# Optimization experiments

Measured on AMD Instinct MI355X. Metric: run time of the kernel, lower is better.

The kernel has to match this reference:

```python
import jax, jax.numpy as jnp
import numpy as np

HEADS = 16

def setup_inputs() -> dict:
    key = jax.random.key(0)
    ks = jax.random.split(key, 5)
    B, T, D = 2, 2048, 2048
    s = 0.02
    return {
        "x": jax.random.normal(ks[0], (B, T, D), dtype=jnp.float32),
        "Wq": jax.random.normal(ks[1], (D, D), dtype=jnp.float32) * s,
        "Wk": jax.random.normal(ks[2], (D, D), dtype=jnp.float32) * s,
        "Wv": jax.random.normal(ks[3], (D, D), dtype=jnp.float32) * s,
        "Wo": jax.random.normal(ks[4], (D, D), dtype=jnp.float32) * s,
    }

def reference(x, Wq, Wk, Wv, Wo):
    B, T, _ = x.shape
    H = HEADS
    Dh = Wq.shape[1] // H
    # projections: [B,T,H,Dh]
    q = (x @ Wq).reshape(B, T, H, Dh)
    k = (x @ Wk).reshape(B, T, H, Dh)
    v = (x @ Wv).reshape(B, T, H, Dh)
    # raw scores [B,H,T,T]
    scores = jnp.einsum("bthd,bshd->bhts", q, k)
    # NOTE (faithful to source): mask is multiplicative 0/1 tril (the
    # masked_fill(-inf) in the torch code is not in-place and has no effect),
    # and the scale is sqrt(token_len), not sqrt(head_dim).
    mask = jnp.tril(jnp.ones((T, T), dtype=scores.dtype))
    scores = scores * mask
    attn = jax.nn.softmax(scores / (T ** 0.5), axis=-1)
    out = jnp.einsum("bhts,bshd->bthd", attn, v).reshape(B, T, H * Dh)
    return out @ Wo
```

## Files before the change

### kernel.cpp

```cpp
#include <hip/hip_runtime.h>


typedef __attribute__((ext_vector_type(4))) float  f32x4;
typedef __attribute__((ext_vector_type(8))) short  bf16x8;
typedef __attribute__((ext_vector_type(4))) unsigned short u16x4;

#define AS1 __attribute__((address_space(1)))
#define AS3 __attribute__((address_space(3)))

__device__ __forceinline__ void llds16(const void* g, void* l) {
  __builtin_amdgcn_global_load_lds((const AS1 void*)g, (AS3 void*)l, 16, 0, 0);
}

__device__ __forceinline__ unsigned short f2bf(float f) {
  unsigned int u = __builtin_bit_cast(unsigned int, f);
  u += 0x7fffu + ((u >> 16) & 1u);
  return (unsigned short)(u >> 16);
}

__device__ __forceinline__ unsigned short f2bfru(float f) {
  return (unsigned short)((__builtin_bit_cast(unsigned int, f) + 0x8000u) >> 16);
}

__device__ __forceinline__ float bf2f(unsigned short u) {
  return __builtin_bit_cast(float, (unsigned int)u << 16);
}

__global__ __launch_bounds__(256) void prep_kernel(
    const float* __restrict__ x,
    const float* __restrict__ W0, const float* __restrict__ W1,
    const float* __restrict__ W2, const float* __restrict__ W3,
    unsigned short* __restrict__ Xb,
    unsigned short* __restrict__ T0, unsigned short* __restrict__ T1,
    unsigned short* __restrict__ T2, unsigned short* __restrict__ T3) {
  __shared__ float tile[32][33];
  const int z = blockIdx.z;
  const int tx = threadIdx.x;
  const int ty = threadIdx.y;
  if (z == 4) {
    int blk = blockIdx.y * 64 + blockIdx.x;
    int t = (ty << 5) + tx;
    int i = blk * 512 + t;
#pragma unroll
    for (int c = 0; c < 2; ++c) {
      f32x4 v = ((const f32x4*)x)[i + (c << 8)];
      u16x4 o;
      o[0] = f2bf(v[0]); o[1] = f2bf(v[1]); o[2] = f2bf(v[2]); o[3] = f2bf(v[3]);
      ((u16x4*)Xb)[i + (c << 8)] = o;
    }
    return;
  }
  const float* W = (z == 0) ? W0 : (z == 1) ? W1 : (z == 2) ? W2 : W3;
  unsigned short* Wt = (z == 0) ? T0 : (z == 1) ? T1 : (z == 2) ? T2 : T3;
  const int bx = blockIdx.x << 5;
  const int by = blockIdx.y << 5;
#pragma unroll
  for (int r = ty; r < 32; r += 8)
    tile[r][tx] = W[(size_t)(bx + r) * 2048 + by + tx];
  __syncthreads();
#pragma unroll
  for (int r = ty; r < 32; r += 8)
    Wt[(size_t)(by + r) * 2048 + bx + tx] = f2bf(tile[tx][r]);
}

__global__ __launch_bounds__(512, 2) void gemm_qkv(const unsigned short* __restrict__ A,
                                                   const unsigned short* __restrict__ Bt,
                                                   unsigned short* __restrict__ Qb,
                                                   unsigned short* __restrict__ Kb,
                                                   unsigned short* __restrict__ Vt) {
  constexpr int SLOT = 49152;
  __shared__ __align__(16) char smem[3 * SLOT];
  const int tid  = threadIdx.x;
  const int lane = tid & 63;
  const int w    = tid >> 6;
  const int wr   = w >> 2;
  const int wc   = w & 3;
  const int q16  = lane >> 4;
  const int l15  = lane & 15;
  const int f    = blockIdx.x;
  const int g    = f >> 3;
  const int bn   = (f & 7) * 3 + (g % 3);
  const int bm   = g / 3;

  const int srow = tid >> 3;
  const int scl  = (tid & 7) ^ (srow & 7);
  const unsigned short* aS = A  + (size_t)((bm << 7) + srow) * 2048 + (scl << 3);
  const unsigned short* bS = Bt + (size_t)(bn * 256 + srow) * 2048 + (scl << 3);
  const int sdst = tid << 4;

  const int swzb = (q16 ^ (l15 & 7)) << 4;
  const int aRd  = ((wr << 6) + l15) << 7;

  f32x4 acc[4][4];
#pragma unroll
  for (int i = 0; i < 4; ++i)
#pragma unroll
    for (int j = 0; j < 4; ++j) acc[i][j] = (f32x4){0.f, 0.f, 0.f, 0.f};

  auto stageT = [&](int kt, char* sb) {
    const size_t ko = (size_t)kt << 6;
    llds16(aS + ko,               sb + sdst);
    llds16(aS + (64 * 2048) + ko, sb + 8192 + sdst);
#pragma unroll
    for (int r = 0; r < 4; ++r)
      llds16(bS + (size_t)r * (64 * 2048) + ko, sb + 16384 + (r << 13) + sdst);
  };

  auto computeT = [&](const char* base) {
#pragma unroll
    for (int ks = 0; ks < 2; ++ks) {
      const int sw = swzb ^ (ks << 6);
      bf16x8 af[4], bf[4];
#pragma unroll
      for (int mi = 0; mi < 4; ++mi)
        af[mi] = *(const bf16x8*)(base + aRd + (mi << 11) + sw);
#pragma unroll
      for (int ni = 0; ni < 4; ++ni)
        bf[ni] = *(const bf16x8*)(base + 16384 + (((wc << 6) + l15) << 7) + (ni << 11) + sw);
      __builtin_amdgcn_s_setprio(1);
#pragma unroll
      for (int mi = 0; mi < 4; ++mi)
#pragma unroll
        for (int ni = 0; ni < 4; ++ni)
          acc[mi][ni] = __builtin_amdgcn_mfma_f32_16x16x32_bf16(af[mi], bf[ni], acc[mi][ni], 0, 0, 0);
      __builtin_amdgcn_s_setprio(0);
    }
  };

  char* s0 = smem;
  char* s1 = smem + SLOT;
  char* s2 = smem + 2 * SLOT;

#define W6()  asm volatile("s_waitcnt vmcnt(6)" ::: "memory")
#define W0()  asm volatile("s_waitcnt vmcnt(0)" ::: "memory")
#define BAR() __builtin_amdgcn_s_barrier()

  stageT(0, s0); stageT(1, s1);
  W6(); BAR();
  stageT(2, s2);
  computeT(s0);
#pragma unroll 1
  for (int b = 1; b <= 25; b += 3) {
    W6(); BAR(); stageT(b + 2, s0); computeT(s1);
    W6(); BAR(); stageT(b + 3, s1); computeT(s2);
    W6(); BAR(); stageT(b + 4, s2); computeT(s0);
  }
  W6(); BAR(); stageT(30, s0); computeT(s1);
  W6(); BAR(); stageT(31, s1); computeT(s2);
  W6(); BAR(); computeT(s0);
  W0(); BAR(); computeT(s1);

#undef W6
#undef W0
#undef BAR

  const float qscale = 0.02209708691207961f;
  const int rb = q16 << 2;
#pragma unroll
  for (int mi = 0; mi < 4; ++mi) {
    int m0 = (bm << 7) + (wr << 6) + (mi << 4) + rb;
#pragma unroll
    for (int ni = 0; ni < 4; ++ni) {
      int gn = (bn << 8) + (wc << 6) + (ni << 4) + l15;
      int region = gn >> 11;
      int nloc = gn & 2047;
      if (region == 0) {
#pragma unroll
        for (int j = 0; j < 4; ++j)
          Qb[(size_t)(m0 + j) * 2048 + nloc] = f2bf(acc[mi][ni][j] * qscale);
      } else if (region == 1) {
#pragma unroll
        for (int j = 0; j < 4; ++j)
          Kb[(size_t)(m0 + j) * 2048 + nloc] = f2bf(acc[mi][ni][j]);
      } else {
        u16x4 pk;
#pragma unroll
        for (int j = 0; j < 4; ++j) pk[j] = f2bf(acc[mi][ni][j]);
        int b = m0 >> 11, t = m0 & 2047;
        *(u16x4*)(Vt + ((size_t)((b << 4) + (nloc >> 7)) * 128 + (nloc & 127)) * 2048 + t) = pk;
      }
    }
  }
}

__global__ __launch_bounds__(256, 2) void gemm_wo(const unsigned short* __restrict__ A,
                                                  const unsigned short* __restrict__ Bt,
                                                  float* __restrict__ Co) {
  constexpr int SLOT = 8192 + 8192;
  __shared__ __align__(16) char smem[3 * SLOT];

  const int tid  = threadIdx.x;
  const int lane = tid & 63;
  const int w    = tid >> 6;
  const int q16  = lane >> 4;
  const int l15  = lane & 15;
  const int f    = blockIdx.x;
  const int g    = f >> 3;
  const int bn   = ((f & 7) << 1) + (g & 1);
  const int bm   = g >> 1;
  const int wmb  = (w >> 1) << 6;
  const int wnb  = (w & 1) << 6;

  f32x4 acc[4][4];
#pragma unroll
  for (int i = 0; i < 4; ++i)
#pragma unroll
    for (int j = 0; j < 4; ++j) acc[i][j] = (f32x4){0.f, 0.f, 0.f, 0.f};

  const int rowA = tid >> 2;
  const int chA  = tid & 3;
  auto stageT = [&](int t, char* sb) {
    const int k0 = t << 5;
#pragma unroll
    for (int r = 0; r < 2; ++r) {
      int row = (r << 6) + rowA;
      const unsigned short* src = A + (size_t)((bm << 7) + row) * 2048 + k0
                                    + ((chA ^ ((row >> 1) & 3)) << 3);
      llds16(src, sb + (r << 12) + (w << 10));
    }
#pragma unroll
    for (int r = 0; r < 2; ++r) {
      int row = (r << 6) + rowA;
      const unsigned short* src = Bt + (size_t)((bn << 7) + row) * 2048 + k0
                                     + ((chA ^ ((row >> 1) & 3)) << 3);
      llds16(src, sb + 8192 + (r << 12) + (w << 10));
    }
  };

  auto computeT = [&](const char* base) {
    bf16x8 af[4], bf[4];
#pragma unroll
    for (int mi = 0; mi < 4; ++mi) {
      int row = wmb + (mi << 4) + l15;
      af[mi] = *(const bf16x8*)(base + (row << 6) + ((q16 ^ ((row >> 1) & 3)) << 4));
    }
#pragma unroll
    for (int ni = 0; ni < 4; ++ni) {
      int row = wnb + (ni << 4) + l15;
      bf[ni] = *(const bf16x8*)(base + 8192 + (row << 6) + ((q16 ^ ((row >> 1) & 3)) << 4));
    }
    __builtin_amdgcn_s_setprio(1);
#pragma unroll
    for (int mi = 0; mi < 4; ++mi)
#pragma unroll
      for (int ni = 0; ni < 4; ++ni)
        acc[mi][ni] = __builtin_amdgcn_mfma_f32_16x16x32_bf16(af[mi], bf[ni], acc[mi][ni], 0, 0, 0);
    __builtin_amdgcn_s_setprio(0);
  };

  auto STEP = [&](int t, char* cbase, char* sbase) {
    asm volatile("s_waitcnt vmcnt(4)" ::: "memory");
    __builtin_amdgcn_s_barrier();
    stageT(t + 2, sbase);
    computeT(cbase);
  };

  char* s0 = smem;
  char* s1 = smem + SLOT;
  char* s2 = smem + 2 * SLOT;

  stageT(0, s0); stageT(1, s1);
#pragma unroll 1
  for (int t = 0; t < 60; t += 3) {
    STEP(t,     s0, s2);
    STEP(t + 1, s1, s0);
    STEP(t + 2, s2, s1);
  }
  STEP(60, s0, s2);
  STEP(61, s1, s0);
  asm volatile("s_waitcnt vmcnt(4)" ::: "memory");
  __builtin_amdgcn_s_barrier();
  computeT(s2);
  asm volatile("s_waitcnt vmcnt(0)" ::: "memory");
  __builtin_amdgcn_s_barrier();
  computeT(s0);

  const int rb = q16 << 2;
#pragma unroll
  for (int mi = 0; mi < 4; ++mi) {
    int m0 = (bm << 7) + wmb + (mi << 4) + rb;
#pragma unroll
    for (int ni = 0; ni < 4; ++ni) {
      int n = (bn << 7) + wnb + (ni << 4) + l15;
#pragma unroll
      for (int j = 0; j < 4; ++j)
        Co[(size_t)(m0 + j) * 2048 + n] = acc[mi][ni][j];
    }
  }
}

__global__ __launch_bounds__(256) void vsuf_kernel(const unsigned short* __restrict__ Vt,
                                                   float* __restrict__ Suf) {
  const int row  = blockIdx.x * 4 + (threadIdx.x >> 6);
  const int lane = threadIdx.x & 63;
  const unsigned short* vp = Vt + (size_t)row * 2048 + (lane << 5);
  float a = 0.f;
#pragma unroll
  for (int c = 0; c < 4; ++c) {
    bf16x8 v = *(const bf16x8*)(vp + (c << 3));
#pragma unroll
    for (int j = 0; j < 8; ++j) a += bf2f((unsigned short)v[j]);
  }
  float I = a;
#pragma unroll
  for (int off = 1; off < 64; off <<= 1) {
    float t = __shfl_down(I, off, 64);
    I += (lane + off < 64) ? t : 0.f;
  }
  Suf[(size_t)lane * 4096 + row] = I;
  if (lane == 0) Suf[(size_t)64 * 4096 + row] = 0.f;
}

__global__ __launch_bounds__(256, 2) void attn_kernel(const unsigned short* __restrict__ Q,
                                                      const unsigned short* __restrict__ K,
                                                      const unsigned short* __restrict__ V,
                                                      const float* __restrict__ Suf,
                                                      unsigned short* __restrict__ O) {
  __shared__ __align__(16) char smem[57344];
  const int tid  = threadIdx.x;
  const int lane = tid & 63;
  const int w    = tid >> 6;
  const int q16  = lane >> 4;
  const int l15  = lane & 15;
  const int f    = blockIdx.x;
  const int bh   = ((f & 7) << 2) + ((f >> 3) & 3);
  const int fs   = f >> 5;
  const int strip = (fs < 8) ? (15 - fs) : (fs - 8);
  const int b  = bh >> 4;
  const size_t qkbase = ((size_t)(b << 11)) * 2048 + ((size_t)(bh & 15) << 7);
  const size_t vbase  = (size_t)bh << 18;
  const int rb = q16 << 2;
  char* Psm = smem + 49152 + (w << 11);

  const int numIter = 4 * strip + 4;
  const int t0 = (strip << 7) + (w << 5);

  auto stage = [&](int s0, int sb) {
#pragma unroll
    for (int c = 0; c < 2; ++c) {
      int ch = (w << 1) + c;
      int rowK = (ch << 2) + q16;
      int colbK = (l15 << 4) ^ ((rowK & 7) << 4);
      llds16(K + qkbase + (size_t)(s0 + rowK) * 2048 + (colbK >> 1), smem + sb + (ch << 10));
      int rowV = (ch << 4) + (lane >> 2);
      int colbV = ((lane & 3) << 4) ^ (((rowV >> 2) & 3) << 4);
      llds16(V + vbase + (size_t)rowV * 2048 + s0 + (colbV >> 1), smem + sb + 8192 + (ch << 10));
    }
  };

  bf16x8 qf[4], qg[4];
  {
    const unsigned short* qp = Q + qkbase + (size_t)(t0 + l15) * 2048 + (q16 << 3);
#pragma unroll
    for (int kk = 0; kk < 4; ++kk) qf[kk] = *(const bf16x8*)(qp + (kk << 5));
    const unsigned short* qp2 = qp + (size_t)16 * 2048;
#pragma unroll
    for (int kk = 0; kk < 4; ++kk) qg[kk] = *(const bf16x8*)(qp2 + (kk << 5));
  }

  f32x4 oA[8], oB[8];
#pragma unroll
  for (int i = 0; i < 8; ++i) { oA[i] = (f32x4){0.f,0.f,0.f,0.f}; oB[i] = (f32x4){0.f,0.f,0.f,0.f}; }
  float ellA[4] = {0.f,0.f,0.f,0.f}, ellB[4] = {0.f,0.f,0.f,0.f};

  stage(0, 0);
  stage(32, 16384);
  asm volatile("s_waitcnt vmcnt(4)" ::: "memory");
  __syncthreads();

  int cs = 0;
  for (int it = 0; it < numIter; ++it) {
    const int s0 = it << 5;
    const bool st = (it + 2 < numIter);
    if (st) {
      int ss = cs + 2; if (ss >= 3) ss -= 3;
      stage(s0 + 64, ss << 14);
    }

    if (s0 <= t0) {
      const int kb = cs << 14;
      const int vb = kb + 8192;

      f32x4 sA = (f32x4){0.f,0.f,0.f,0.f}, sB = sA, sC = sA, sD = sA;
#pragma unroll
      for (int kk = 0; kk < 4; ++kk) {
        int r0 = l15, r1 = 16 + l15;
        bf16x8 k0f = *(const bf16x8*)(smem + kb + (r0 << 8) + (((kk << 6) + (q16 << 4)) ^ ((r0 & 7) << 4)));
        bf16x8 k1f = *(const bf16x8*)(smem + kb + (r1 << 8) + (((kk << 6) + (q16 << 4)) ^ ((r1 & 7) << 4)));
        sA = __builtin_amdgcn_mfma_f32_16x16x32_bf16(qf[kk], k0f, sA, 0, 0, 0);
        sC = __builtin_amdgcn_mfma_f32_16x16x32_bf16(qg[kk], k0f, sC, 0, 0, 0);
        sB = __builtin_amdgcn_mfma_f32_16x16x32_bf16(qf[kk], k1f, sB, 0, 0, 0);
        sD = __builtin_amdgcn_mfma_f32_16x16x32_bf16(qg[kk], k1f, sD, 0, 0, 0);
      }

      float pA[4], pB[4], pC[4], pD[4];
      if (s0 + 32 <= t0) {
#pragma unroll
        for (int j = 0; j < 4; ++j) {
          pA[j] = __expf(sA[j]); pB[j] = __expf(sB[j]);
          pC[j] = __expf(sC[j]); pD[j] = __expf(sD[j]);
          ellA[j] += pA[j] + pB[j];
          ellB[j] += pC[j] + pD[j];
        }
      } else {
#pragma unroll
        for (int j = 0; j < 4; ++j) {
          int tA = t0 + rb + j, tB = tA + 16;
          int sa = s0 + l15;
          float vA = (sa <= tA)      ? sA[j] : 0.f;
          float vB = (sa + 16 <= tA) ? sB[j] : 0.f;
          float vC = (sa <= tB)      ? sC[j] : 0.f;
          float vD = (sa + 16 <= tB) ? sD[j] : 0.f;
          pA[j] = __expf(vA); pB[j] = __expf(vB);
          pC[j] = __expf(vC); pD[j] = __expf(vD);
          ellA[j] += pA[j] + pB[j];
          ellB[j] += pC[j] + pD[j];
        }
      }

#pragma unroll
      for (int j = 0; j < 4; ++j) {
        int rA = rb + j;
        int swzA = ((rA >> 1) & 3) << 4;
        *(unsigned short*)(Psm + (rA << 6) + ((l15 << 1) ^ swzA))        = f2bfru(pA[j]);
        *(unsigned short*)(Psm + (rA << 6) + ((32 + (l15 << 1)) ^ swzA)) = f2bfru(pB[j]);
        int rB = rA + 16;
        int swzB = ((rB >> 1) & 3) << 4;
        *(unsigned short*)(Psm + (rB << 6) + ((l15 << 1) ^ swzB))        = f2bfru(pC[j]);
        *(unsigned short*)(Psm + (rB << 6) + ((32 + (l15 << 1)) ^ swzB)) = f2bfru(pD[j]);
      }
      asm volatile("s_waitcnt lgkmcnt(0)" ::: "memory");

      bf16x8 paA, paB;
      {
        int r = l15;
        paA = *(const bf16x8*)(Psm + (r << 6) + ((q16 << 4) ^ (((r >> 1) & 3) << 4)));
        int r2 = 16 + l15;
        paB = *(const bf16x8*)(Psm + (r2 << 6) + ((q16 << 4) ^ (((r2 >> 1) & 3) << 4)));
      }
#pragma unroll
      for (int ni = 0; ni < 8; ++ni) {
        int dr = (ni << 4) + l15;
        bf16x8 vbf = *(const bf16x8*)(smem + vb + (dr << 6) + ((q16 << 4) ^ (((dr >> 2) & 3) << 4)));
        oA[ni] = __builtin_amdgcn_mfma_f32_16x16x32_bf16(paA, vbf, oA[ni], 0, 0, 0);
        oB[ni] = __builtin_amdgcn_mfma_f32_16x16x32_bf16(paB, vbf, oB[ni], 0, 0, 0);
      }
    }

    if (it + 1 < numIter) {
      if (st) asm volatile("s_waitcnt vmcnt(4)" ::: "memory");
      else    asm volatile("s_waitcnt vmcnt(0)" ::: "memory");
      __builtin_amdgcn_s_barrier();
    }
    cs = (cs + 1 == 3) ? 0 : cs + 1;
  }

  const int send = t0 + 32;
  const float* sp = Suf + (size_t)(send >> 5) * 4096 + ((size_t)bh << 7);
  const float extra = (float)(2048 - send);
#pragma unroll
  for (int ni = 0; ni < 8; ++ni) {
    float sv = sp[(ni << 4) + l15];
#pragma unroll
    for (int j = 0; j < 4; ++j) { oA[ni][j] += sv; oB[ni][j] += sv; }
  }

#pragma unroll
  for (int j = 0; j < 4; ++j) {
    float r = ellA[j];
    r += __shfl_xor(r, 1, 64);
    r += __shfl_xor(r, 2, 64);
    r += __shfl_xor(r, 4, 64);
    r += __shfl_xor(r, 8, 64);
    float inv = 1.0f / (r + extra);
    int t = t0 + rb + j;
    unsigned short* op = O + qkbase + (size_t)t * 2048;
#pragma unroll
    for (int ni = 0; ni < 8; ++ni)
      op[(ni << 4) + l15] = f2bf(oA[ni][j] * inv);

    float r2 = ellB[j];
    r2 += __shfl_xor(r2, 1, 64);
    r2 += __shfl_xor(r2, 2, 64);
    r2 += __shfl_xor(r2, 4, 64);
    r2 += __shfl_xor(r2, 8, 64);
    float inv2 = 1.0f / (r2 + extra);
    unsigned short* op2 = op + (size_t)16 * 2048;
#pragma unroll
    for (int ni = 0; ni < 8; ++ni)
      op2[(ni << 4) + l15] = f2bf(oB[ni][j] * inv2);
  }
}

extern "C" void kernel_launch(void* const* d_in, const int* in_sizes, int n_in,
                              void* d_out, int out_size, void* d_ws, size_t ws_size,
                              hipStream_t stream) {
  (void)in_sizes; (void)n_in; (void)out_size; (void)ws_size;
  const float* x  = (const float*)d_in[0];
  const float* Wq = (const float*)d_in[1];
  const float* Wk = (const float*)d_in[2];
  const float* Wv = (const float*)d_in[3];
  const float* Wo = (const float*)d_in[4];
  float* out = (float*)d_out;

  char* ws = (char*)d_ws;
  unsigned short* Xb  = (unsigned short*)(ws);
  unsigned short* Wqt = (unsigned short*)(ws + 16777216);
  unsigned short* Wkt = (unsigned short*)(ws + 16777216 + 8388608);
  unsigned short* Wvt = (unsigned short*)(ws + 16777216 + 2 * 8388608);
  unsigned short* Wot = (unsigned short*)(ws + 16777216 + 3 * 8388608);
  unsigned short* Qb  = (unsigned short*)(ws + 50331648);
  unsigned short* Kb  = (unsigned short*)(ws + 67108864);
  unsigned short* Vt  = (unsigned short*)(ws + 83886080);
  unsigned short* Ob  = Xb;
  float*          Suf = (float*)Wqt;

  {
    dim3 tb(32, 8), tg(64, 64, 5);
    prep_kernel<<<tg, tb, 0, stream>>>(x, Wq, Wk, Wv, Wo, Xb, Wqt, Wkt, Wvt, Wot);
  }
  gemm_qkv<<<768, 512, 0, stream>>>(Xb, Wqt, Qb, Kb, Vt);

  vsuf_kernel<<<1024, 256, 0, stream>>>(Vt, Suf);

  attn_kernel<<<512, 256, 0, stream>>>(Qb, Kb, Vt, Suf, Ob);

  gemm_wo<<<512, 256, 0, stream>>>(Ob, Wot, out);
}
```

Measured before the change: 260.6 us.

## Load V tiles directly into registers with double-buffered prefetch, shrink LDS

V tiles now go straight from global memory into registers through a two-slot register double buffer, instead of being staged into LDS and read back. Only K is still staged in LDS, which cuts shared memory from 56KB to 32KB. The main loop is manually unrolled by two so the two V register buffers can alternate. The aim is to remove LDS traffic and the V-tile LDS reads, and possibly to raise occupancy. In exchange, register pressure grows (16 extra bf16x8 vectors) and V global loads are per-lane strided rather than LDS-coalesced. The odd-count tail is handled implicitly, because numIter is always a multiple of 4.

```diff
diff --git a/kernel.cpp b/kernel.cpp
--- a/kernel.cpp
+++ b/kernel.cpp
@@ -316,7 +316,7 @@
                                                       const unsigned short* __restrict__ V,
                                                       const float* __restrict__ Suf,
                                                       unsigned short* __restrict__ O) {
-  __shared__ __align__(16) char smem[57344];
+  __shared__ __align__(16) char smem[32768];
   const int tid  = threadIdx.x;
   const int lane = tid & 63;
   const int w    = tid >> 6;
@@ -328,25 +328,30 @@
   const int strip = (fs < 8) ? (15 - fs) : (fs - 8);
   const int b  = bh >> 4;
   const size_t qkbase = ((size_t)(b << 11)) * 2048 + ((size_t)(bh & 15) << 7);
-  const size_t vbase  = (size_t)bh << 18;
   const int rb = q16 << 2;
-  char* Psm = smem + 49152 + (w << 11);
+  char* Psm = smem + 24576 + (w << 11);
 
   const int numIter = 4 * strip + 4;
   const int t0 = (strip << 7) + (w << 5);
 
-  auto stage = [&](int s0, int sb) {
-#pragma unroll
-    for (int c = 0; c < 2; ++c) {
-      int ch = (w << 1) + c;
-      int rowK = (ch << 2) + q16;
-      int colbK = (l15 << 4) ^ ((rowK & 7) << 4);
-      llds16(K + qkbase + (size_t)(s0 + rowK) * 2048 + (colbK >> 1), smem + sb + (ch << 10));
-      int rowV = (ch << 4) + (lane >> 2);
-      int colbV = ((lane & 3) << 4) ^ (((rowV >> 2) & 3) << 4);
-      llds16(V + vbase + (size_t)rowV * 2048 + s0 + (colbV >> 1), smem + sb + 8192 + (ch << 10));
-    }
-  };
+  const unsigned short* vSrc = V + ((size_t)bh << 18) + (size_t)l15 * 2048 + (q16 << 3);
+
+#define LOADV(S0_, D)  do {                                                  \
+    _Pragma("unroll")                                                        \
+    for (int ni = 0; ni < 8; ++ni)                                           \
+      D[ni] = *(const bf16x8*)(vSrc + (size_t)ni * 32768 + (S0_));           \
+  } while (0)
+
+#define STAGEK(S0_, SB) do {                                                 \
+    _Pragma("unroll")                                                        \
+    for (int c = 0; c < 2; ++c) {                                            \
+      int ch = (w << 1) + c;                                                 \
+      int rowK = (ch << 2) + q16;                                            \
+      int colbK = (l15 << 4) ^ ((rowK & 7) << 4);                            \
+      llds16(K + qkbase + (size_t)((S0_) + rowK) * 2048 + (colbK >> 1),      \
+             (SB) + (ch << 10));                                             \
+    }                                                                        \
+  } while (0)
 
   bf16x8 qf[4], qg[4];
   {
@@ -362,98 +367,107 @@
 #pragma unroll
   for (int i = 0; i < 8; ++i) { oA[i] = (f32x4){0.f,0.f,0.f,0.f}; oB[i] = (f32x4){0.f,0.f,0.f,0.f}; }
   float ellA[4] = {0.f,0.f,0.f,0.f}, ellB[4] = {0.f,0.f,0.f,0.f};
-
-  stage(0, 0);
-  stage(32, 16384);
-  asm volatile("s_waitcnt vmcnt(4)" ::: "memory");
+  bf16x8 vA[8], vB[8];
+
+#define TILE(T, KSLOT, KSTG, VUSE, VLD) do {                                 \
+    const int s0_ = (T) << 5;                                                \
+    const bool hasNext_  = ((T) + 1 < numIter);                              \
+    const bool hasStage_ = ((T) + 2 < numIter);                              \
+    if (hasNext_)  LOADV(s0_ + 32, VLD);                                     \
+    if (hasStage_) STAGEK(s0_ + 64, KSTG);                                   \
+    if (s0_ <= t0) {                                                         \
+      const char* kb_ = (KSLOT);                                             \
+      f32x4 sA = (f32x4){0.f,0.f,0.f,0.f}, sB = sA, sC = sA, sD = sA;        \
+      _Pragma("unroll")                                                      \
+      for (int kk = 0; kk < 4; ++kk) {                                       \
+        int r0 = l15, r1 = 16 + l15;                                         \
+        bf16x8 k0f = *(const bf16x8*)(kb_ + (r0 << 8) +                      \
+                     (((kk << 6) + (q16 << 4)) ^ ((r0 & 7) << 4)));          \
+        bf16x8 k1f = *(const bf16x8*)(kb_ + (r1 << 8) +                      \
+                     (((kk << 6) + (q16 << 4)) ^ ((r1 & 7) << 4)));          \
+        sA = __builtin_amdgcn_mfma_f32_16x16x32_bf16(qf[kk], k0f, sA, 0, 0, 0); \
+        sC = __builtin_amdgcn_mfma_f32_16x16x32_bf16(qg[kk], k0f, sC, 0, 0, 0); \
+        sB = __builtin_amdgcn_mfma_f32_16x16x32_bf16(qf[kk], k1f, sB, 0, 0, 0); \
+        sD = __builtin_amdgcn_mfma_f32_16x16x32_bf16(qg[kk], k1f, sD, 0, 0, 0); \
+      }                                                                      \
+      float pA[4], pB[4], pC[4], pD[4];                                      \
+      if (s0_ + 32 <= t0) {                                                  \
+        _Pragma("unroll")                                                    \
+        for (int j = 0; j < 4; ++j) {                                        \
+          pA[j] = __expf(sA[j]); pB[j] = __expf(sB[j]);                      \
+          pC[j] = __expf(sC[j]); pD[j] = __expf(sD[j]);                      \
+          ellA[j] += pA[j] + pB[j];                                          \
+          ellB[j] += pC[j] + pD[j];                                          \
+        }                                                                    \
+      } else {                                                               \
+        _Pragma("unroll")                                                    \
+        for (int j = 0; j < 4; ++j) {                                        \
+          int tA = t0 + rb + j, tB = tA + 16;                                \
+          int sa = s0_ + l15;                                                \
+          float vA_ = (sa <= tA)      ? sA[j] : 0.f;                         \
+          float vB_ = (sa + 16 <= tA) ? sB[j] : 0.f;                         \
+          float vC_ = (sa <= tB)      ? sC[j] : 0.f;                         \
+          float vD_ = (sa + 16 <= tB) ? sD[j] : 0.f;                         \
+          pA[j] = __expf(vA_); pB[j] = __expf(vB_);                          \
+          pC[j] = __expf(vC_); pD[j] = __expf(vD_);                          \
+          ellA[j] += pA[j] + pB[j];                                          \
+          ellB[j] += pC[j] + pD[j];                                          \
+        }                                                                    \
+      }                                                                      \
+      _Pragma("unroll")                                                      \
+      for (int j = 0; j < 4; ++j) {                                          \
+        int rA = rb + j;                                                     \
+        int swzA = ((rA >> 1) & 3) << 4;                                     \
+        *(unsigned short*)(Psm + (rA << 6) + ((l15 << 1) ^ swzA))        = f2bfru(pA[j]); \
+        *(unsigned short*)(Psm + (rA << 6) + ((32 + (l15 << 1)) ^ swzA)) = f2bfru(pB[j]); \
+        int rB = rA + 16;                                                    \
+        int swzB = ((rB >> 1) & 3) << 4;                                     \
+        *(unsigned short*)(Psm + (rB << 6) + ((l15 << 1) ^ swzB))        = f2bfru(pC[j]); \
+        *(unsigned short*)(Psm + (rB << 6) + ((32 + (l15 << 1)) ^ swzB)) = f2bfru(pD[j]); \
+      }                                                                      \
+      asm volatile("s_waitcnt lgkmcnt(0)" ::: "memory");                     \
+      bf16x8 paA, paB;                                                       \
+      {                                                                      \
+        int r = l15;                                                         \
+        paA = *(const bf16x8*)(Psm + (r << 6) + ((q16 << 4) ^ (((r >> 1) & 3) << 4)));  \
+        int r2 = 16 + l15;                                                   \
+        paB = *(const bf16x8*)(Psm + (r2 << 6) + ((q16 << 4) ^ (((r2 >> 1) & 3) << 4))); \
+      }                                                                      \
+      _Pragma("unroll")                                                      \
+      for (int ni = 0; ni < 8; ++ni) {                                       \
+        oA[ni] = __builtin_amdgcn_mfma_f32_16x16x32_bf16(paA, VUSE[ni], oA[ni], 0, 0, 0); \
+        oB[ni] = __builtin_amdgcn_mfma_f32_16x16x32_bf16(paB, VUSE[ni], oB[ni], 0, 0, 0); \
+      }                                                                      \
+    }                                                                        \
+    if (hasNext_) {                                                          \
+      if (hasStage_) asm volatile("s_waitcnt vmcnt(2)" ::: "memory");        \
+      else           asm volatile("s_waitcnt vmcnt(0)" ::: "memory");        \
+      __builtin_amdgcn_s_barrier();                                          \
+    }                                                                        \
+  } while (0)
+
+  STAGEK(0, smem);
+  STAGEK(32, smem + 8192);
+  LOADV(0, vA);
+  asm volatile("s_waitcnt vmcnt(0)" ::: "memory");
   __syncthreads();
 
-  int cs = 0;
-  for (int it = 0; it < numIter; ++it) {
-    const int s0 = it << 5;
-    const bool st = (it + 2 < numIter);
-    if (st) {
-      int ss = cs + 2; if (ss >= 3) ss -= 3;
-      stage(s0 + 64, ss << 14);
-    }
-
-    if (s0 <= t0) {
-      const int kb = cs << 14;
-      const int vb = kb + 8192;
-
-      f32x4 sA = (f32x4){0.f,0.f,0.f,0.f}, sB = sA, sC = sA, sD = sA;
-#pragma unroll
-      for (int kk = 0; kk < 4; ++kk) {
-        int r0 = l15, r1 = 16 + l15;
-        bf16x8 k0f = *(const bf16x8*)(smem + kb + (r0 << 8) + (((kk << 6) + (q16 << 4)) ^ ((r0 & 7) << 4)));
-        bf16x8 k1f = *(const bf16x8*)(smem + kb + (r1 << 8) + (((kk << 6) + (q16 << 4)) ^ ((r1 & 7) << 4)));
-        sA = __builtin_amdgcn_mfma_f32_16x16x32_bf16(qf[kk], k0f, sA, 0, 0, 0);
-        sC = __builtin_amdgcn_mfma_f32_16x16x32_bf16(qg[kk], k0f, sC, 0, 0, 0);
-        sB = __builtin_amdgcn_mfma_f32_16x16x32_bf16(qf[kk], k1f, sB, 0, 0, 0);
-        sD = __builtin_amdgcn_mfma_f32_16x16x32_bf16(qg[kk], k1f, sD, 0, 0, 0);
-      }
-
-      float pA[4], pB[4], pC[4], pD[4];
-      if (s0 + 32 <= t0) {
-#pragma unroll
-        for (int j = 0; j < 4; ++j) {
-          pA[j] = __expf(sA[j]); pB[j] = __expf(sB[j]);
-          pC[j] = __expf(sC[j]); pD[j] = __expf(sD[j]);
-          ellA[j] += pA[j] + pB[j];
-          ellB[j] += pC[j] + pD[j];
-        }
-      } else {
-#pragma unroll
-        for (int j = 0; j < 4; ++j) {
-          int tA = t0 + rb + j, tB = tA + 16;
-          int sa = s0 + l15;
-          float vA = (sa <= tA)      ? sA[j] : 0.f;
-          float vB = (sa + 16 <= tA) ? sB[j] : 0.f;
-          float vC = (sa <= tB)      ? sC[j] : 0.f;
-          float vD = (sa + 16 <= tB) ? sD[j] : 0.f;
-          pA[j] = __expf(vA); pB[j] = __expf(vB);
-          pC[j] = __expf(vC); pD[j] = __expf(vD);
-          ellA[j] += pA[j] + pB[j];
-          ellB[j] += pC[j] + pD[j];
-        }
-      }
-
-#pragma unroll
-      for (int j = 0; j < 4; ++j) {
-        int rA = rb + j;
-        int swzA = ((rA >> 1) & 3) << 4;
-        *(unsigned short*)(Psm + (rA << 6) + ((l15 << 1) ^ swzA))        = f2bfru(pA[j]);
-        *(unsigned short*)(Psm + (rA << 6) + ((32 + (l15 << 1)) ^ swzA)) = f2bfru(pB[j]);
-        int rB = rA + 16;
-        int swzB = ((rB >> 1) & 3) << 4;
-        *(unsigned short*)(Psm + (rB << 6) + ((l15 << 1) ^ swzB))        = f2bfru(pC[j]);
-        *(unsigned short*)(Psm + (rB << 6) + ((32 + (l15 << 1)) ^ swzB)) = f2bfru(pD[j]);
-      }
-      asm volatile("s_waitcnt lgkmcnt(0)" ::: "memory");
-
-      bf16x8 paA, paB;
-      {
-        int r = l15;
-        paA = *(const bf16x8*)(Psm + (r << 6) + ((q16 << 4) ^ (((r >> 1) & 3) << 4)));
-        int r2 = 16 + l15;
-        paB = *(const bf16x8*)(Psm + (r2 << 6) + ((q16 << 4) ^ (((r2 >> 1) & 3) << 4)));
-      }
-#pragma unroll
-      for (int ni = 0; ni < 8; ++ni) {
-        int dr = (ni << 4) + l15;
-        bf16x8 vbf = *(const bf16x8*)(smem + vb + (dr << 6) + ((q16 << 4) ^ (((dr >> 2) & 3) << 4)));
-        oA[ni] = __builtin_amdgcn_mfma_f32_16x16x32_bf16(paA, vbf, oA[ni], 0, 0, 0);
-        oB[ni] = __builtin_amdgcn_mfma_f32_16x16x32_bf16(paB, vbf, oB[ni], 0, 0, 0);
-      }
-    }
-
-    if (it + 1 < numIter) {
-      if (st) asm volatile("s_waitcnt vmcnt(4)" ::: "memory");
-      else    asm volatile("s_waitcnt vmcnt(0)" ::: "memory");
-      __builtin_amdgcn_s_barrier();
-    }
-    cs = (cs + 1 == 3) ? 0 : cs + 1;
-  }
+  int csl = 0;
+#pragma unroll 1
+  for (int it = 0; it < numIter; it += 2) {
+    int c1 = csl + 1; if (c1 >= 3) c1 -= 3;
+    int c2 = csl + 2; if (c2 >= 3) c2 -= 3;
+    char* sl0 = smem + (csl << 13);
+    char* sl1 = smem + (c1 << 13);
+    char* sl2 = smem + (c2 << 13);
+    TILE(it,     sl0, sl2, vA, vB);
+    TILE(it + 1, sl1, sl0, vB, vA);
+    csl = c2;
+  }
+
+#undef TILE
+#undef LOADV
+#undef STAGEK
 
   const int send = t0 + 32;
   const float* sp = Suf + (size_t)(send >> 5) * 4096 + ((size_t)bh << 7);
```

After: 309.6 us. +18.8%, slower.
